# Kernel optimization log

Hardware: AMD Instinct MI355X
Metric: run time of the kernel (lower is better)

## Reference

```python
import jax, jax.numpy as jnp
import numpy as np

HEADS = 4
HEAD_DIM = 32
SCALE = HEAD_DIM ** (-0.5)


def setup_inputs() -> dict:
    key = jax.random.key(0)
    k1, k2, k3, k4 = jax.random.split(key, 4)
    x = jax.random.normal(k1, (32, 256, 64, 64), dtype=jnp.float32)
    # to_qkv: Conv2d(256 -> 3*heads*head_dim=384, kernel 1x1, bias=False)
    w_qkv = jax.random.normal(k2, (384, 256), dtype=jnp.float32) * 0.02
    # to_out: Conv2d(128 -> 256, kernel 1x1, bias=True)
    w_out = jax.random.normal(k3, (256, 128), dtype=jnp.float32) * 0.02
    b_out = jax.random.normal(k4, (256,), dtype=jnp.float32) * 0.02
    return {"x": x, "w_qkv": w_qkv, "w_out": w_out, "b_out": b_out}


def reference(x, w_qkv, w_out, b_out):
    b, c, H, W = x.shape
    n = H * W
    # 1x1 conv == channel matmul; produce (b, 3, heads, head_dim, n)
    qkv = jnp.einsum('oc,bchw->bohw', w_qkv, x).reshape(b, 3, HEADS, HEAD_DIM, n)
    q, k, v = qkv[:, 0], qkv[:, 1], qkv[:, 2]  # each (b, h, d, n)
    q = jax.nn.softmax(q, axis=-1) * SCALE     # softmax over spatial n
    k = jax.nn.softmax(k, axis=-2)             # softmax over channel d
    # context: (b, h, e, d) -- reduce over n
    context = jnp.einsum('bhen,bhdn->bhed', k, v)
    # out: (b, h, d, n)
    out = jnp.einsum('bhed,bhen->bhdn', context, q)
    out = out.reshape(b, HEADS * HEAD_DIM, H, W)
    # to_out 1x1 conv with bias
    return jnp.einsum('oc,bchw->bohw', w_out, out) + b_out[None, :, None, None]
```

## Files before the change

### kernel.cpp

```cpp
#include <hip/hip_runtime.h>
#include <hip/hip_bf16.h>

#define NTOK 4096
#define SCALE 0.17677669529663687f

using f32x4 = __attribute__((ext_vector_type(4))) float;
using s16x8 = __attribute__((ext_vector_type(8))) short;

__device__ __forceinline__ ushort bf_rne(float f) {
  unsigned int u = __builtin_bit_cast(unsigned int, f);
  u += 0x7FFFu + ((u >> 16) & 1u);
  return (ushort)(u >> 16);
}
__device__ __forceinline__ void gl_lds16(const ushort* g, ushort* l) {
  __builtin_amdgcn_global_load_lds(
      (const __attribute__((address_space(1))) unsigned int*)g,
      (__attribute__((address_space(3))) unsigned int*)l, 16, 0, 0);
}

__global__ __launch_bounds__(256) void k_cvt_w(const float* __restrict__ w,
                                               ushort* __restrict__ wb) {
  const int i = blockIdx.x * 256 + threadIdx.x;
  const float4 v = reinterpret_cast<const float4*>(w)[i];
  ushort4 h;
  h.x = bf_rne(v.x); h.y = bf_rne(v.y); h.z = bf_rne(v.z); h.w = bf_rne(v.w);
  reinterpret_cast<ushort4*>(wb)[i] = h;
}

__global__ __launch_bounds__(256) void k_cvt_x(const float* __restrict__ x,
                                               ushort* __restrict__ xT) {
  const int n0 = blockIdx.x * 64;
  const int c0 = blockIdx.y * 128;
  const int b  = blockIdx.z;
  __shared__ ushort T[64 * 136];
  const int t = threadIdx.x;
  const int rr = t >> 4;
  const int nq = t & 15;
  const float* xp = x + ((size_t)b * 256 + c0) * NTOK + n0;
#pragma unroll
  for (int p = 0; p < 8; ++p) {
    const int c = p * 16 + rr;
    const float4 v = *reinterpret_cast<const float4*>(xp + (size_t)c * NTOK + nq * 4);
    T[(nq * 4 + 0) * 136 + c] = bf_rne(v.x);
    T[(nq * 4 + 1) * 136 + c] = bf_rne(v.y);
    T[(nq * 4 + 2) * 136 + c] = bf_rne(v.z);
    T[(nq * 4 + 3) * 136 + c] = bf_rne(v.w);
  }
  __syncthreads();
  ushort* op = xT + ((size_t)b * NTOK + n0) * 256 + c0;
#pragma unroll
  for (int i = 0; i < 4; ++i) {
    const int row = i * 16 + rr;
    *reinterpret_cast<uint4*>(op + (size_t)row * 256 + nq * 8) =
        *reinterpret_cast<const uint4*>(&T[row * 136 + nq * 8]);
  }
}

__global__ __launch_bounds__(256) void k_qkv_mfma(const ushort* __restrict__ xT,
                                                  const ushort* __restrict__ wb,
                                                  ushort* __restrict__ Ecn,
                                                  ushort* __restrict__ kb,
                                                  ushort* __restrict__ vb,
                                                  float* __restrict__ spart) {
  const int n0 = blockIdx.x * 128;
  const int o0 = blockIdx.y * 128;
  const int b  = blockIdx.z;
  const ushort* xTb = xT + (size_t)b * NTOK * 256;

  __shared__ ushort As[8192];
  __shared__ ushort Bs[8192];

  const int t = threadIdx.x;
  const int lane = t & 63;
  const int wv = t >> 6;
  const int wr = wv >> 1, wc = wv & 1;
  const int lm = lane & 15;
  const int lk = lane >> 4;

  int aoff[4][2], boff[4][2];
#pragma unroll
  for (int mf = 0; mf < 4; ++mf) {
    const int ar = wr * 64 + mf * 16 + lm;
#pragma unroll
    for (int ks = 0; ks < 2; ++ks)
      aoff[mf][ks] = ar * 64 + 8 * ((ks * 4 + lk) ^ (ar & 7));
  }
#pragma unroll
  for (int nf = 0; nf < 4; ++nf) {
    const int br = wc * 64 + nf * 16 + lm;
#pragma unroll
    for (int ks = 0; ks < 2; ++ks)
      boff[nf][ks] = br * 64 + 8 * ((ks * 4 + lk) ^ (br & 7));
  }
  size_t gaA[4], gaB[4];
  int lb[4];
#pragma unroll
  for (int i = 0; i < 4; ++i) {
    const int s_total = t + 256 * i;
    const int r = s_total >> 3;
    const int q = (s_total & 7) ^ (r & 7);
    gaA[i] = (size_t)(o0 + r) * 256 + q * 8;
    gaB[i] = (size_t)(n0 + r) * 256 + q * 8;
    lb[i] = wv * 512 + i * 2048;
  }

  f32x4 acc[4][4];
#pragma unroll
  for (int i = 0; i < 4; ++i)
#pragma unroll
    for (int j = 0; j < 4; ++j) acc[i][j] = (f32x4){0.f, 0.f, 0.f, 0.f};

  for (int it = 0; it < 4; ++it) {
    const size_t c0 = (size_t)it * 64;
#pragma unroll
    for (int i = 0; i < 4; ++i) {
      gl_lds16(wb + gaA[i] + c0, As + lb[i]);
      gl_lds16(xTb + gaB[i] + c0, Bs + lb[i]);
    }
    __syncthreads();
#pragma unroll
    for (int ks = 0; ks < 2; ++ks) {
      s16x8 af[4], bf[4];
#pragma unroll
      for (int mf = 0; mf < 4; ++mf)
        af[mf] = *reinterpret_cast<const s16x8*>(As + aoff[mf][ks]);
#pragma unroll
      for (int nf = 0; nf < 4; ++nf)
        bf[nf] = *reinterpret_cast<const s16x8*>(Bs + boff[nf][ks]);
#pragma unroll
      for (int mf = 0; mf < 4; ++mf)
#pragma unroll
        for (int nf = 0; nf < 4; ++nf)
          acc[mf][nf] = __builtin_amdgcn_mfma_f32_16x16x32_bf16(af[mf], bf[nf], acc[mf][nf], 0, 0, 0);
    }
    __syncthreads();
  }

  if (blockIdx.y == 0) {
    ushort* C = Ecn + (size_t)b * 128 * NTOK + n0;
    float* sp = spart + (((size_t)b * 32 + blockIdx.x) * 2 + wc) * 128;
#pragma unroll
    for (int mf = 0; mf < 4; ++mf) {
#pragma unroll
      for (int r = 0; r < 4; ++r) {
        const int ch = wr * 64 + mf * 16 + lk * 4 + r;
        float s = 0.f;
#pragma unroll
        for (int nf = 0; nf < 4; ++nf) {
          const float e = __expf(acc[mf][nf][r]);
          s += e;
          C[(size_t)ch * NTOK + wc * 64 + nf * 16 + lm] = bf_rne(e);
        }
        s += __shfl_xor(s, 1, 64);
        s += __shfl_xor(s, 2, 64);
        s += __shfl_xor(s, 4, 64);
        s += __shfl_xor(s, 8, 64);
        if (lm == 0) sp[ch] = s;
      }
    }
  } else if (blockIdx.y == 1) {
#pragma unroll
    for (int nf = 0; nf < 4; ++nf) {
#pragma unroll
      for (int g = 0; g < 2; ++g) {
        float m = -1e30f;
#pragma unroll
        for (int mm = 0; mm < 2; ++mm)
#pragma unroll
          for (int r = 0; r < 4; ++r)
            m = fmaxf(m, acc[g * 2 + mm][nf][r]);
        m = fmaxf(m, __shfl_xor(m, 16, 64));
        m = fmaxf(m, __shfl_xor(m, 32, 64));
        float s = 0.f;
#pragma unroll
        for (int mm = 0; mm < 2; ++mm)
#pragma unroll
          for (int r = 0; r < 4; ++r) {
            const float e = __expf(acc[g * 2 + mm][nf][r] - m);
            acc[g * 2 + mm][nf][r] = e;
            s += e;
          }
        s += __shfl_xor(s, 16, 64);
        s += __shfl_xor(s, 32, 64);
        const float inv = 1.0f / s;
#pragma unroll
        for (int mm = 0; mm < 2; ++mm)
#pragma unroll
          for (int r = 0; r < 4; ++r) acc[g * 2 + mm][nf][r] *= inv;
      }
    }
    ushort* C = kb + (size_t)b * 128 * NTOK + n0;
#pragma unroll
    for (int mf = 0; mf < 4; ++mf) {
      const int row0 = wr * 64 + mf * 16 + lk * 4;
#pragma unroll
      for (int nf = 0; nf < 4; ++nf) {
        const int col = wc * 64 + nf * 16 + lm;
#pragma unroll
        for (int r = 0; r < 4; ++r)
          C[(size_t)(row0 + r) * NTOK + col] = bf_rne(acc[mf][nf][r]);
      }
    }
  } else {
    ushort* C = vb + (size_t)b * 128 * NTOK + n0;
#pragma unroll
    for (int mf = 0; mf < 4; ++mf) {
      const int row0 = wr * 64 + mf * 16 + lk * 4;
#pragma unroll
      for (int nf = 0; nf < 4; ++nf) {
        const int col = wc * 64 + nf * 16 + lm;
#pragma unroll
        for (int r = 0; r < 4; ++r)
          C[(size_t)(row0 + r) * NTOK + col] = bf_rne(acc[mf][nf][r]);
      }
    }
  }
}

__global__ __launch_bounds__(256) void k_context_mfma(const ushort* __restrict__ kb,
                                                      const ushort* __restrict__ vb,
                                                      float* __restrict__ ctx_part) {
  const int bh = blockIdx.x;
  const int w = threadIdx.x >> 6;
  const int lane = threadIdx.x & 63;
  const int lm = lane & 15, lk = lane >> 4;
  const ushort* kp = kb + (size_t)bh * 32 * NTOK + (size_t)w * 1024;
  const ushort* vp = vb + (size_t)bh * 32 * NTOK + (size_t)w * 1024;
  f32x4 acc[2][2];
#pragma unroll
  for (int i = 0; i < 2; ++i)
#pragma unroll
    for (int j = 0; j < 2; ++j) acc[i][j] = (f32x4){0.f, 0.f, 0.f, 0.f};
#pragma unroll 4
  for (int ks = 0; ks < 32; ++ks) {
    const int coff = ks * 32 + lk * 8;
    const s16x8 a0 = *reinterpret_cast<const s16x8*>(kp + (size_t)lm * NTOK + coff);
    const s16x8 a1 = *reinterpret_cast<const s16x8*>(kp + (size_t)(16 + lm) * NTOK + coff);
    const s16x8 b0 = *reinterpret_cast<const s16x8*>(vp + (size_t)lm * NTOK + coff);
    const s16x8 b1 = *reinterpret_cast<const s16x8*>(vp + (size_t)(16 + lm) * NTOK + coff);
    acc[0][0] = __builtin_amdgcn_mfma_f32_16x16x32_bf16(a0, b0, acc[0][0], 0, 0, 0);
    acc[0][1] = __builtin_amdgcn_mfma_f32_16x16x32_bf16(a0, b1, acc[0][1], 0, 0, 0);
    acc[1][0] = __builtin_amdgcn_mfma_f32_16x16x32_bf16(a1, b0, acc[1][0], 0, 0, 0);
    acc[1][1] = __builtin_amdgcn_mfma_f32_16x16x32_bf16(a1, b1, acc[1][1], 0, 0, 0);
  }
  float* op = ctx_part + ((size_t)bh * 4 + w) * 1024;
#pragma unroll
  for (int et = 0; et < 2; ++et)
#pragma unroll
    for (int dt = 0; dt < 2; ++dt)
#pragma unroll
      for (int r = 0; r < 4; ++r)
        op[(et * 16 + lk * 4 + r) * 32 + dt * 16 + lm] = acc[et][dt][r];
}

__global__ __launch_bounds__(256) void k_w2(const float* __restrict__ ctx_part,
                                            const float* __restrict__ spart,
                                            const float* __restrict__ w_out,
                                            ushort* __restrict__ W2b) {
  const int b = blockIdx.x;
  const int t = threadIdx.x;
  __shared__ float ctx[4096];
  __shared__ float fbuf[128];
#pragma unroll
  for (int i = 0; i < 16; ++i) {
    const int idx = t + 256 * i;
    const int h = idx >> 10, ed = idx & 1023;
    const float* cp = ctx_part + ((size_t)((b * 4 + h) * 4)) * 1024 + ed;
    ctx[idx] = cp[0] + cp[1024] + cp[2048] + cp[3072];
  }
  if (t < 128) {
    float s = 0.f;
    for (int p = 0; p < 64; ++p) s += spart[((size_t)b * 64 + p) * 128 + t];
    fbuf[t] = SCALE / s;
  }
  __syncthreads();
  const float* wrow = w_out + (size_t)t * 128;
  ushort* wout_row = W2b + ((size_t)b * 256 + t) * 128;
  float wv[32];
  for (int h = 0; h < 4; ++h) {
#pragma unroll
    for (int d = 0; d < 32; ++d) wv[d] = wrow[h * 32 + d];
#pragma unroll 4
    for (int e = 0; e < 32; ++e) {
      float a = 0.f;
#pragma unroll
      for (int d = 0; d < 32; ++d) a += wv[d] * ctx[h * 1024 + e * 32 + d];
      wout_row[h * 32 + e] = bf_rne(a * fbuf[h * 32 + e]);
    }
  }
}

__global__ __launch_bounds__(256) void k_out_mfma(const ushort* __restrict__ Ecn,
                                                  const ushort* __restrict__ W2b,
                                                  const float* __restrict__ b_out,
                                                  float* __restrict__ out) {
  const int n0 = blockIdx.x * 128;
  const int o0 = blockIdx.y * 128;
  const int b  = blockIdx.z;
  const ushort* A  = W2b + (size_t)b * 256 * 128;
  const ushort* Bq = Ecn + (size_t)b * 128 * NTOK;

  __shared__ ushort As[8192];
  __shared__ ushort Bt[8192];

  const int t = threadIdx.x;
  const int lane = t & 63;
  const int wv = t >> 6;
  const int wr = wv >> 1, wc = wv & 1;
  const int lm = lane & 15;
  const int lk = lane >> 4;

  int aoff[4][2], boff[4][2];
#pragma unroll
  for (int mf = 0; mf < 4; ++mf) {
    const int ar = wr * 64 + mf * 16 + lm;
#pragma unroll
    for (int ks = 0; ks < 2; ++ks)
      aoff[mf][ks] = ar * 64 + 8 * ((ks * 4 + lk) ^ (ar & 7));
  }
#pragma unroll
  for (int nf = 0; nf < 4; ++nf) {
    const int br = wc * 64 + nf * 16 + lm;
#pragma unroll
    for (int ks = 0; ks < 2; ++ks)
      boff[nf][ks] = br * 64 + 8 * ((ks * 4 + lk) ^ (br & 7));
  }
  size_t gaA[4];
  int lb[4];
#pragma unroll
  for (int i = 0; i < 4; ++i) {
    const int s_total = t + 256 * i;
    const int r = s_total >> 3;
    const int q = (s_total & 7) ^ (r & 7);
    gaA[i] = (size_t)(o0 + r) * 128 + q * 8;
    lb[i] = wv * 512 + i * 2048;
  }
  int bst[8], bn[8], bcg[8];
#pragma unroll
  for (int i = 0; i < 8; ++i) {
    const int u = t + 256 * i;
    bn[i] = u & 127;
    bcg[i] = u >> 7;
    bst[i] = bn[i] * 64 + 8 * ((bcg[i] >> 1) ^ (bn[i] & 7)) + (bcg[i] & 1) * 4;
  }

  f32x4 acc[4][4];
#pragma unroll
  for (int i = 0; i < 4; ++i)
#pragma unroll
    for (int j = 0; j < 4; ++j) acc[i][j] = (f32x4){0.f, 0.f, 0.f, 0.f};

  for (int it = 0; it < 2; ++it) {
    const size_t c0 = (size_t)it * 64;
    __syncthreads();
#pragma unroll
    for (int i = 0; i < 4; ++i)
      gl_lds16(A + gaA[i] + c0, As + lb[i]);
#pragma unroll
    for (int i = 0; i < 8; ++i) {
      const ushort* gp = Bq + (c0 + bcg[i] * 4) * NTOK + n0 + bn[i];
      ushort4 hvec;
      hvec.x = gp[0];
      hvec.y = gp[NTOK];
      hvec.z = gp[2 * NTOK];
      hvec.w = gp[3 * NTOK];
      *reinterpret_cast<ushort4*>(Bt + bst[i]) = hvec;
    }
    __syncthreads();
#pragma unroll
    for (int ks = 0; ks < 2; ++ks) {
      s16x8 af[4], bf[4];
#pragma unroll
      for (int mf = 0; mf < 4; ++mf)
        af[mf] = *reinterpret_cast<const s16x8*>(As + aoff[mf][ks]);
#pragma unroll
      for (int nf = 0; nf < 4; ++nf)
        bf[nf] = *reinterpret_cast<const s16x8*>(Bt + boff[nf][ks]);
#pragma unroll
      for (int mf = 0; mf < 4; ++mf)
#pragma unroll
        for (int nf = 0; nf < 4; ++nf)
          acc[mf][nf] = __builtin_amdgcn_mfma_f32_16x16x32_bf16(af[mf], bf[nf], acc[mf][nf], 0, 0, 0);
    }
  }

  float* C = out + ((size_t)b * 256 + o0) * NTOK + n0;
#pragma unroll
  for (int mf = 0; mf < 4; ++mf) {
    const int row0 = wr * 64 + mf * 16 + lk * 4;
#pragma unroll
    for (int nf = 0; nf < 4; ++nf) {
      const int col = wc * 64 + nf * 16 + lm;
#pragma unroll
      for (int r = 0; r < 4; ++r) {
        const float bias = b_out[o0 + row0 + r];
        C[(size_t)(row0 + r) * NTOK + col] = acc[mf][nf][r] + bias;
      }
    }
  }
}

extern "C" void kernel_launch(void* const* d_in, const int* in_sizes, int n_in,
                              void* d_out, int out_size, void* d_ws, size_t ws_size,
                              hipStream_t stream) {
  const float* x     = (const float*)d_in[0];
  const float* w_qkv = (const float*)d_in[1];
  const float* w_out = (const float*)d_in[2];
  const float* b_out = (const float*)d_in[3];
  float* out = (float*)d_out;

  ushort* xT  = (ushort*)d_ws;
  ushort* kb  = xT + (size_t)33554432;
  ushort* vb  = kb + (size_t)16777216;
  ushort* Ecn = vb + (size_t)16777216;
  float*  ctx_part = (float*)(Ecn + (size_t)16777216);
  float*  spart    = ctx_part + 524288;
  ushort* wb  = (ushort*)(spart + 262144);
  ushort* W2b = wb + 98304;

  k_cvt_w<<<96, 256, 0, stream>>>(w_qkv, wb);
  k_cvt_x<<<dim3(64, 2, 32), 256, 0, stream>>>(x, xT);
  k_qkv_mfma<<<dim3(32, 3, 32), 256, 0, stream>>>(xT, wb, Ecn, kb, vb, spart);
  k_context_mfma<<<128, 256, 0, stream>>>(kb, vb, ctx_part);
  k_w2<<<32, 256, 0, stream>>>(ctx_part, spart, w_out, W2b);
  k_out_mfma<<<dim3(32, 2, 32), 256, 0, stream>>>(Ecn, W2b, b_out, out);
}
```

Before: 189.0 us.

## Double-buffer LDS tiles in QKV GEMM with narrower K-steps and new swizzle

The QKV projection GEMM now splits K into eight 32-wide steps instead of four 64-wide steps. It ping-pongs between two LDS buffers so the next tile's global-to-LDS load is issued before the current tile's MFMAs. A new XOR swizzle matches the 32-element row stride. The goal is to overlap memory latency with compute and drop one barrier per iteration, at the cost of twice as many loop iterations and barriers overall.

```diff
diff --git a/kernel.cpp b/kernel.cpp
--- a/kernel.cpp
+++ b/kernel.cpp
@@ -3,6 +3,8 @@
 
 #define NTOK 4096
 #define SCALE 0.17677669529663687f
+
+#define SWZ(r) ((((r) >> 1) ^ ((r) >> 3)) & 3)
 
 using f32x4 = __attribute__((ext_vector_type(4))) float;
 using s16x8 = __attribute__((ext_vector_type(8))) short;
@@ -67,8 +69,8 @@
   const int b  = blockIdx.z;
   const ushort* xTb = xT + (size_t)b * NTOK * 256;
 
-  __shared__ ushort As[8192];
-  __shared__ ushort Bs[8192];
+  __shared__ ushort As[2 * 4096];
+  __shared__ ushort Bs[2 * 4096];
 
   const int t = threadIdx.x;
   const int lane = t & 63;
@@ -77,32 +79,26 @@
   const int lm = lane & 15;
   const int lk = lane >> 4;
 
-  int aoff[4][2], boff[4][2];
+  int aoff[4], boff[4];
 #pragma unroll
   for (int mf = 0; mf < 4; ++mf) {
     const int ar = wr * 64 + mf * 16 + lm;
-#pragma unroll
-    for (int ks = 0; ks < 2; ++ks)
-      aoff[mf][ks] = ar * 64 + 8 * ((ks * 4 + lk) ^ (ar & 7));
+    aoff[mf] = ar * 32 + 8 * (lk ^ SWZ(ar));
   }
 #pragma unroll
   for (int nf = 0; nf < 4; ++nf) {
     const int br = wc * 64 + nf * 16 + lm;
-#pragma unroll
-    for (int ks = 0; ks < 2; ++ks)
-      boff[nf][ks] = br * 64 + 8 * ((ks * 4 + lk) ^ (br & 7));
-  }
-  size_t gaA[4], gaB[4];
-  int lb[4];
-#pragma unroll
-  for (int i = 0; i < 4; ++i) {
-    const int s_total = t + 256 * i;
-    const int r = s_total >> 3;
-    const int q = (s_total & 7) ^ (r & 7);
-    gaA[i] = (size_t)(o0 + r) * 256 + q * 8;
-    gaB[i] = (size_t)(n0 + r) * 256 + q * 8;
-    lb[i] = wv * 512 + i * 2048;
-  }
+    boff[nf] = br * 32 + 8 * (lk ^ SWZ(br));
+  }
+  const int s1 = t, s2 = t + 256;
+  const int r1 = s1 >> 2, q1 = (s1 & 3) ^ SWZ(r1);
+  const int r2 = s2 >> 2, q2 = (s2 & 3) ^ SWZ(r2);
+  const size_t ga1 = (size_t)(o0 + r1) * 256 + q1 * 8;
+  const size_t ga2 = (size_t)(o0 + r2) * 256 + q2 * 8;
+  const size_t gb1 = (size_t)(n0 + r1) * 256 + q1 * 8;
+  const size_t gb2 = (size_t)(n0 + r2) * 256 + q2 * 8;
+  const int lbase1 = wv * 512;
+  const int lbase2 = 2048 + wv * 512;
 
   f32x4 acc[4][4];
 #pragma unroll
@@ -110,29 +106,34 @@
 #pragma unroll
     for (int j = 0; j < 4; ++j) acc[i][j] = (f32x4){0.f, 0.f, 0.f, 0.f};
 
-  for (int it = 0; it < 4; ++it) {
-    const size_t c0 = (size_t)it * 64;
-#pragma unroll
-    for (int i = 0; i < 4; ++i) {
-      gl_lds16(wb + gaA[i] + c0, As + lb[i]);
-      gl_lds16(xTb + gaB[i] + c0, Bs + lb[i]);
-    }
-    __syncthreads();
-#pragma unroll
-    for (int ks = 0; ks < 2; ++ks) {
-      s16x8 af[4], bf[4];
-#pragma unroll
-      for (int mf = 0; mf < 4; ++mf)
-        af[mf] = *reinterpret_cast<const s16x8*>(As + aoff[mf][ks]);
+  gl_lds16(wb + ga1, As + lbase1);
+  gl_lds16(wb + ga2, As + lbase2);
+  gl_lds16(xTb + gb1, Bs + lbase1);
+  gl_lds16(xTb + gb2, Bs + lbase2);
+  __syncthreads();
+
+  for (int it = 0; it < 8; ++it) {
+    const int cb = (it & 1) * 4096;
+    if (it < 7) {
+      const int nb = ((it + 1) & 1) * 4096;
+      const size_t c1 = (size_t)(it + 1) * 32;
+      gl_lds16(wb + ga1 + c1, As + nb + lbase1);
+      gl_lds16(wb + ga2 + c1, As + nb + lbase2);
+      gl_lds16(xTb + gb1 + c1, Bs + nb + lbase1);
+      gl_lds16(xTb + gb2 + c1, Bs + nb + lbase2);
+    }
+    s16x8 af[4], bf[4];
+#pragma unroll
+    for (int mf = 0; mf < 4; ++mf)
+      af[mf] = *reinterpret_cast<const s16x8*>(As + cb + aoff[mf]);
+#pragma unroll
+    for (int nf = 0; nf < 4; ++nf)
+      bf[nf] = *reinterpret_cast<const s16x8*>(Bs + cb + boff[nf]);
+#pragma unroll
+    for (int mf = 0; mf < 4; ++mf)
 #pragma unroll
       for (int nf = 0; nf < 4; ++nf)
-        bf[nf] = *reinterpret_cast<const s16x8*>(Bs + boff[nf][ks]);
-#pragma unroll
-      for (int mf = 0; mf < 4; ++mf)
-#pragma unroll
-        for (int nf = 0; nf < 4; ++nf)
-          acc[mf][nf] = __builtin_amdgcn_mfma_f32_16x16x32_bf16(af[mf], bf[nf], acc[mf][nf], 0, 0, 0);
-    }
+        acc[mf][nf] = __builtin_amdgcn_mfma_f32_16x16x32_bf16(af[mf], bf[nf], acc[mf][nf], 0, 0, 0);
     __syncthreads();
   }
 
```

Result: slower. 195.3 us (+3.3%).
